# Optimization experiments

Hardware: AMD Instinct MI355X
Metric: run time of the kernel (lower is better)

## Reference

```python
import jax, jax.numpy as jnp
import numpy as np

TASKS = 32768          # init kwarg `tasks`
N_HEADS = TASKS + 1    # tasks + 1 distilled/shared head
IN_DIM, HID, OUT = 3, 100, 5


def setup_inputs() -> dict:
    key = jax.random.key(0)
    kx, k1, kb1, k2, kb2 = jax.random.split(key, 5)
    # per-task stacked parameters (equivalent to ModuleList of Linears)
    x = jax.random.normal(kx, (N_HEADS, IN_DIM), dtype=jnp.float32)
    # init scale ~ PyTorch default: U(-1/sqrt(fan_in), 1/sqrt(fan_in)); gaussian approx fine
    W1 = jax.random.normal(k1, (N_HEADS, HID, IN_DIM), dtype=jnp.float32) * (1.0 / np.sqrt(IN_DIM))
    b1 = jax.random.normal(kb1, (N_HEADS, HID), dtype=jnp.float32) * (1.0 / np.sqrt(IN_DIM))
    W2 = jax.random.normal(k2, (N_HEADS, OUT, HID), dtype=jnp.float32) * (1.0 / np.sqrt(HID))
    b2 = jax.random.normal(kb2, (N_HEADS, OUT), dtype=jnp.float32) * (1.0 / np.sqrt(HID))
    return {"x": x, "W1": W1, "b1": b1, "W2": W2, "b2": b2}


def reference(x, W1, b1, W2, b2):
    # x: (T+1, 3) -- one state vector per task head (matches x.view(tasks+1, -1))
    T1 = W1.shape[0]
    x = x.reshape(T1, -1)                                   # (T+1, 3)
    h = jax.nn.relu(jnp.einsum('thi,ti->th', W1, x) + b1)   # (T+1, 100)
    logits = jnp.einsum('toh,th->to', W2, h) + b2           # (T+1, 5)
    return jax.nn.softmax(logits, axis=-1)                  # (T+1, 5)
```

## Files before the change

### kernel.cpp

```cpp
#include <hip/hip_runtime.h>
#include <math.h>


#define N_HEADS 32769
#define HID     100
#define OUT     5

#define HEADS_PER_BLOCK 4
#define FLOATS_PER_HEAD 400
#define LDS_B1 300

#define GLOBAL_AS __attribute__((address_space(1)))
#define LDS_AS    __attribute__((address_space(3)))

static __device__ __forceinline__ void async_copy16(const void* g, void* l) {
    __builtin_amdgcn_global_load_lds((const GLOBAL_AS void*)g, (LDS_AS void*)l,
                                     16, 0, 0);
}

template <int CTRL, int ROW_MASK>
static __device__ __forceinline__ float dpp_add_step(float acc) {
    union { float f; int i; } in, out;
    in.f = acc;
    out.i = __builtin_amdgcn_update_dpp(0, in.i, CTRL, ROW_MASK, 0xF, false);
    return acc + out.f;
}

static __device__ __forceinline__ float wave_reduce_add(float acc) {
    acc = dpp_add_step<0x111, 0xF>(acc);
    acc = dpp_add_step<0x112, 0xF>(acc);
    acc = dpp_add_step<0x114, 0xF>(acc);
    acc = dpp_add_step<0x118, 0xF>(acc);
    acc = dpp_add_step<0x142, 0xA>(acc);
    acc = dpp_add_step<0x143, 0xC>(acc);
    union { float f; int i; } v, r;
    v.f = acc;
    r.i = __builtin_amdgcn_readlane(v.i, 63);
    return r.f;
}

__global__ __launch_bounds__(256) void distral_kernel(
    const float* __restrict__ x,
    const float* __restrict__ W1,
    const float* __restrict__ b1,
    const float* __restrict__ W2,
    const float* __restrict__ b2,
    float* __restrict__ out)
{
    __shared__ float lds[HEADS_PER_BLOCK * FLOATS_PER_HEAD];

    const int wave = threadIdx.x >> 6;
    const int lane = threadIdx.x & 63;
    const int head = blockIdx.x * HEADS_PER_BLOCK + wave;
    if (head >= N_HEADS) return;

    float* region = lds + wave * FLOATS_PER_HEAD;

    const float* W1h = W1 + (size_t)head * 300;
    const float* b1h = b1 + (size_t)head * 100;
    async_copy16(W1h + 4 * lane,           region);
    if (lane < 11)
        async_copy16(W1h + 256 + 4 * lane, region + 256);
    if (lane < 25)
        async_copy16(b1h + 4 * lane,       region + LDS_B1);

    const float* W2h = W2 + (size_t)head * 500;
    const bool has2 = (lane < HID - 64);

    float w2a[OUT], w2b[OUT] = {0.f, 0.f, 0.f, 0.f, 0.f};
#pragma unroll
    for (int o = 0; o < OUT; ++o)
        w2a[o] = W2h[o * HID + lane];
    if (has2) {
#pragma unroll
        for (int o = 0; o < OUT; ++o)
            w2b[o] = W2h[o * HID + 64 + lane];
    }

    const float x0 = x[head * 3 + 0];
    const float x1 = x[head * 3 + 1];
    const float x2 = x[head * 3 + 2];
    float b2v[OUT];
#pragma unroll
    for (int o = 0; o < OUT; ++o) b2v[o] = b2[head * OUT + o];

    __builtin_amdgcn_s_waitcnt(0x0F70);
    asm volatile("" ::: "memory");

    float h0, h1 = 0.0f;
    {
        const float* r = region + 3 * lane;
        h0 = fmaxf(fmaf(r[0], x0, fmaf(r[1], x1, fmaf(r[2], x2,
                   region[LDS_B1 + lane]))), 0.0f);
    }
    if (has2) {
        const float* r = region + 3 * (lane + 64);
        h1 = fmaxf(fmaf(r[0], x0, fmaf(r[1], x1, fmaf(r[2], x2,
                   region[LDS_B1 + lane + 64]))), 0.0f);
    }

    float logit[OUT];
#pragma unroll
    for (int o = 0; o < OUT; ++o) {
        float p = fmaf(w2b[o], h1, w2a[o] * h0);
        logit[o] = wave_reduce_add(p) + b2v[o];
    }

    float m = -INFINITY;
#pragma unroll
    for (int o = 0; o < OUT; ++o) m = fmaxf(m, logit[o]);
    float e[OUT], s = 0.0f;
#pragma unroll
    for (int o = 0; o < OUT; ++o) { e[o] = __expf(logit[o] - m); s += e[o]; }
    const float inv = 1.0f / s;

    if (lane < OUT) {
        float v = (lane == 0) ? e[0]
                : (lane == 1) ? e[1]
                : (lane == 2) ? e[2]
                : (lane == 3) ? e[3]
                :               e[4];
        out[(size_t)head * OUT + lane] = v * inv;
    }
}

extern "C" void kernel_launch(void* const* d_in, const int* in_sizes, int n_in,
                              void* d_out, int out_size, void* d_ws, size_t ws_size,
                              hipStream_t stream) {
    const float* x  = (const float*)d_in[0];
    const float* W1 = (const float*)d_in[1];
    const float* b1 = (const float*)d_in[2];
    const float* W2 = (const float*)d_in[3];
    const float* b2 = (const float*)d_in[4];
    float* out = (float*)d_out;

    const int blocks = (N_HEADS + HEADS_PER_BLOCK - 1) / HEADS_PER_BLOCK;
    distral_kernel<<<blocks, 256, 0, stream>>>(x, W1, b1, W2, b2, out);
}
```

Baseline: 142.8 us.

## Use persistent waves with register double-buffered prefetch instead of LDS staging

Replaces the one-head-per-wave launch with a fixed grid of 8192 waves that loop over heads, prefetching the next head's weights into registers while the current head is computed. It also drops the LDS async-copy path and loads W1/b1 directly into registers with strided scalar loads. The goal is to hide global memory latency and cut launch and LDS overhead, at the cost of higher register pressure and less coalesced W1 loads (stride-3 per lane).

Result: no change. 145.0 us (+1.5%).

```diff
diff --git a/kernel.cpp b/kernel.cpp
--- a/kernel.cpp
+++ b/kernel.cpp
@@ -5,17 +5,47 @@
 #define N_HEADS 32769
 #define HID     100
 #define OUT     5
+#define NWAVES  8192
 
-#define HEADS_PER_BLOCK 4
-#define FLOATS_PER_HEAD 400
-#define LDS_B1 300
+struct Batch {
+    float w1a0, w1a1, w1a2;
+    float w1b0, w1b1, w1b2;
+    float b1a, b1b;
+    float w2a[OUT], w2b[OUT];
+    float x0, x1, x2;
+    float b2v[OUT];
+};
 
-#define GLOBAL_AS __attribute__((address_space(1)))
-#define LDS_AS    __attribute__((address_space(3)))
+static __device__ __forceinline__ Batch load_batch(
+    const float* __restrict__ x,  const float* __restrict__ W1,
+    const float* __restrict__ b1, const float* __restrict__ W2,
+    const float* __restrict__ b2, int head, int lane)
+{
+    Batch t;
+    const float* W1h = W1 + (size_t)head * 300;
+    const float* b1h = b1 + (size_t)head * 100;
+    const float* W2h = W2 + (size_t)head * 500;
+    const int j2 = (lane + 64 < HID) ? (lane + 64) : (HID - 1);
 
-static __device__ __forceinline__ void async_copy16(const void* g, void* l) {
-    __builtin_amdgcn_global_load_lds((const GLOBAL_AS void*)g, (LDS_AS void*)l,
-                                     16, 0, 0);
+    t.w1a0 = W1h[3 * lane + 0];
+    t.w1a1 = W1h[3 * lane + 1];
+    t.w1a2 = W1h[3 * lane + 2];
+    t.w1b0 = W1h[3 * j2 + 0];
+    t.w1b1 = W1h[3 * j2 + 1];
+    t.w1b2 = W1h[3 * j2 + 2];
+    t.b1a  = b1h[lane];
+    t.b1b  = b1h[j2];
+#pragma unroll
+    for (int o = 0; o < OUT; ++o) {
+        t.w2a[o] = W2h[o * HID + lane];
+        t.w2b[o] = W2h[o * HID + j2];
+    }
+    t.x0 = x[head * 3 + 0];
+    t.x1 = x[head * 3 + 1];
+    t.x2 = x[head * 3 + 2];
+#pragma unroll
+    for (int o = 0; o < OUT; ++o) t.b2v[o] = b2[head * OUT + o];
+    return t;
 }
 
 template <int CTRL, int ROW_MASK>
@@ -39,71 +69,22 @@
     return r.f;
 }
 
-__global__ __launch_bounds__(256) void distral_kernel(
-    const float* __restrict__ x,
-    const float* __restrict__ W1,
-    const float* __restrict__ b1,
-    const float* __restrict__ W2,
-    const float* __restrict__ b2,
-    float* __restrict__ out)
+static __device__ __forceinline__ void process(
+    const Batch& t, int head, int lane, float* __restrict__ out)
 {
-    __shared__ float lds[HEADS_PER_BLOCK * FLOATS_PER_HEAD];
-
-    const int wave = threadIdx.x >> 6;
-    const int lane = threadIdx.x & 63;
-    const int head = blockIdx.x * HEADS_PER_BLOCK + wave;
-    if (head >= N_HEADS) return;
-
-    float* region = lds + wave * FLOATS_PER_HEAD;
-
-    const float* W1h = W1 + (size_t)head * 300;
-    const float* b1h = b1 + (size_t)head * 100;
-    async_copy16(W1h + 4 * lane,           region);
-    if (lane < 11)
-        async_copy16(W1h + 256 + 4 * lane, region + 256);
-    if (lane < 25)
-        async_copy16(b1h + 4 * lane,       region + LDS_B1);
-
-    const float* W2h = W2 + (size_t)head * 500;
     const bool has2 = (lane < HID - 64);
 
-    float w2a[OUT], w2b[OUT] = {0.f, 0.f, 0.f, 0.f, 0.f};
-#pragma unroll
-    for (int o = 0; o < OUT; ++o)
-        w2a[o] = W2h[o * HID + lane];
-    if (has2) {
-#pragma unroll
-        for (int o = 0; o < OUT; ++o)
-            w2b[o] = W2h[o * HID + 64 + lane];
-    }
-
-    const float x0 = x[head * 3 + 0];
-    const float x1 = x[head * 3 + 1];
-    const float x2 = x[head * 3 + 2];
-    float b2v[OUT];
-#pragma unroll
-    for (int o = 0; o < OUT; ++o) b2v[o] = b2[head * OUT + o];
-
-    __builtin_amdgcn_s_waitcnt(0x0F70);
-    asm volatile("" ::: "memory");
-
-    float h0, h1 = 0.0f;
-    {
-        const float* r = region + 3 * lane;
-        h0 = fmaxf(fmaf(r[0], x0, fmaf(r[1], x1, fmaf(r[2], x2,
-                   region[LDS_B1 + lane]))), 0.0f);
-    }
-    if (has2) {
-        const float* r = region + 3 * (lane + 64);
-        h1 = fmaxf(fmaf(r[0], x0, fmaf(r[1], x1, fmaf(r[2], x2,
-                   region[LDS_B1 + lane + 64]))), 0.0f);
-    }
+    float h0 = fmaxf(fmaf(t.w1a0, t.x0, fmaf(t.w1a1, t.x1,
+                     fmaf(t.w1a2, t.x2, t.b1a))), 0.0f);
+    float h1 = fmaxf(fmaf(t.w1b0, t.x0, fmaf(t.w1b1, t.x1,
+                     fmaf(t.w1b2, t.x2, t.b1b))), 0.0f);
+    h1 = has2 ? h1 : 0.0f;
 
     float logit[OUT];
 #pragma unroll
     for (int o = 0; o < OUT; ++o) {
-        float p = fmaf(w2b[o], h1, w2a[o] * h0);
-        logit[o] = wave_reduce_add(p) + b2v[o];
+        float p = fmaf(t.w2b[o], h1, t.w2a[o] * h0);
+        logit[o] = wave_reduce_add(p) + t.b2v[o];
     }
 
     float m = -INFINITY;
@@ -124,6 +105,35 @@
     }
 }
 
+__global__ __launch_bounds__(256) void distral_kernel(
+    const float* __restrict__ x,
+    const float* __restrict__ W1,
+    const float* __restrict__ b1,
+    const float* __restrict__ W2,
+    const float* __restrict__ b2,
+    float* __restrict__ out)
+{
+    const int lane = threadIdx.x & 63;
+    const int w    = (blockIdx.x << 2) | (threadIdx.x >> 6);
+
+    int head  = w;
+    Batch cur = load_batch(x, W1, b1, W2, b2, head, lane);
+
+    for (;;) {
+        const int next  = head + NWAVES;
+        const bool more = (next < N_HEADS);
+        Batch nxt;
+        if (more)
+            nxt = load_batch(x, W1, b1, W2, b2, next, lane);
+
+        process(cur, head, lane, out);
+
+        if (!more) break;
+        cur  = nxt;
+        head = next;
+    }
+}
+
 extern "C" void kernel_launch(void* const* d_in, const int* in_sizes, int n_in,
                               void* d_out, int out_size, void* d_ws, size_t ws_size,
                               hipStream_t stream) {
@@ -134,6 +144,5 @@
     const float* b2 = (const float*)d_in[4];
     float* out = (float*)d_out;
 
-    const int blocks = (N_HEADS + HEADS_PER_BLOCK - 1) / HEADS_PER_BLOCK;
-    distral_kernel<<<blocks, 256, 0, stream>>>(x, W1, b1, W2, b2, out);
+    distral_kernel<<<NWAVES / 4, 256, 0, stream>>>(x, W1, b1, W2, b2, out);
 }
```

## Use persistent waves with double-buffered async LDS staging of all head parameters

Applied to the files above, without the earlier changes.

Replaces the one-head-per-wave launch with a persistent grid of 2816 two-wave blocks. Each wave loops over heads and prefetches the next head's W1, b1, W2, x and b2 into a second LDS buffer while computing the current one. W2, x and b2 now also go through global-to-LDS async copies rather than direct register loads. The aim is to hide memory latency and cut launch and scheduling overhead, at the cost of fewer resident waves, more LDS per wave, and one redundant staging copy on each wave's final iteration.

Result: slower. 146.9 us (+2.9%).

```diff
diff --git a/kernel.cpp b/kernel.cpp
--- a/kernel.cpp
+++ b/kernel.cpp
@@ -6,16 +6,45 @@
 #define HID     100
 #define OUT     5
 
-#define HEADS_PER_BLOCK 4
-#define FLOATS_PER_HEAD 400
-#define LDS_B1 300
+#define WAVES_PER_BLOCK 2
+#define NBLOCKS 2816
+#define NW      (NBLOCKS * WAVES_PER_BLOCK)
+
+#define RSTRIDE 912
+#define OF_B1   300
+#define OF_W2   400
+#define OF_X    900
+#define OF_B2   903
 
 #define GLOBAL_AS __attribute__((address_space(1)))
 #define LDS_AS    __attribute__((address_space(3)))
 
-static __device__ __forceinline__ void async_copy16(const void* g, void* l) {
+static __device__ __forceinline__ void dma16(const void* g, void* l) {
     __builtin_amdgcn_global_load_lds((const GLOBAL_AS void*)g, (LDS_AS void*)l,
                                      16, 0, 0);
+}
+static __device__ __forceinline__ void dma4(const void* g, void* l) {
+    __builtin_amdgcn_global_load_lds((const GLOBAL_AS void*)g, (LDS_AS void*)l,
+                                     4, 0, 0);
+}
+
+static __device__ __forceinline__ void stage_head(
+    int head, int lane, float* region,
+    const float* __restrict__ x,  const float* __restrict__ W1,
+    const float* __restrict__ b1, const float* __restrict__ W2,
+    const float* __restrict__ b2)
+{
+    const float* W1h = W1 + (size_t)head * 300;
+    const float* b1h = b1 + (size_t)head * 100;
+    const float* W2h = W2 + (size_t)head * 500;
+
+    dma16(W1h + 4 * lane,                 region);
+    if (lane < 11) dma16(W1h + 256 + 4 * lane, region + 256);
+    if (lane < 25) dma16(b1h + 4 * lane,  region + OF_B1);
+    dma16(W2h + 4 * lane,                 region + OF_W2);
+    if (lane < 61) dma16(W2h + 256 + 4 * lane, region + OF_W2 + 256);
+    if (lane < 3)  dma4(x + (size_t)head * 3 + lane, region + OF_X);
+    if (lane < 5)  dma4(b2 + (size_t)head * 5 + lane, region + OF_B2);
 }
 
 template <int CTRL, int ROW_MASK>
@@ -25,7 +54,6 @@
     out.i = __builtin_amdgcn_update_dpp(0, in.i, CTRL, ROW_MASK, 0xF, false);
     return acc + out.f;
 }
-
 static __device__ __forceinline__ float wave_reduce_add(float acc) {
     acc = dpp_add_step<0x111, 0xF>(acc);
     acc = dpp_add_step<0x112, 0xF>(acc);
@@ -39,7 +67,7 @@
     return r.f;
 }
 
-__global__ __launch_bounds__(256) void distral_kernel(
+__global__ __launch_bounds__(128) void distral_kernel(
     const float* __restrict__ x,
     const float* __restrict__ W1,
     const float* __restrict__ b1,
@@ -47,80 +75,76 @@
     const float* __restrict__ b2,
     float* __restrict__ out)
 {
-    __shared__ float lds[HEADS_PER_BLOCK * FLOATS_PER_HEAD];
+    __shared__ float lds[WAVES_PER_BLOCK][2][RSTRIDE];
 
-    const int wave = threadIdx.x >> 6;
     const int lane = threadIdx.x & 63;
-    const int head = blockIdx.x * HEADS_PER_BLOCK + wave;
-    if (head >= N_HEADS) return;
+    const int wv   = threadIdx.x >> 6;
+    const int w    = blockIdx.x * WAVES_PER_BLOCK + wv;
 
-    float* region = lds + wave * FLOATS_PER_HEAD;
+    int head = w;
+    stage_head(head, lane, &lds[wv][0][0], x, W1, b1, W2, b2);
 
-    const float* W1h = W1 + (size_t)head * 300;
-    const float* b1h = b1 + (size_t)head * 100;
-    async_copy16(W1h + 4 * lane,           region);
-    if (lane < 11)
-        async_copy16(W1h + 256 + 4 * lane, region + 256);
-    if (lane < 25)
-        async_copy16(b1h + 4 * lane,       region + LDS_B1);
+    int buf = 0;
+    for (;;) {
+        const int  nh   = head + NW;
+        const bool more = (nh < N_HEADS);
+        const int  lh   = more ? nh : w;
+        stage_head(lh, lane, &lds[wv][buf ^ 1][0], x, W1, b1, W2, b2);
 
-    const float* W2h = W2 + (size_t)head * 500;
-    const bool has2 = (lane < HID - 64);
+        asm volatile("" ::: "memory");
+        __builtin_amdgcn_s_waitcnt(0x0F77);
+        asm volatile("" ::: "memory");
 
-    float w2a[OUT], w2b[OUT] = {0.f, 0.f, 0.f, 0.f, 0.f};
+        const float* region = &lds[wv][buf][0];
+
+        const float x0 = region[OF_X + 0];
+        const float x1 = region[OF_X + 1];
+        const float x2 = region[OF_X + 2];
+
+        const bool has2 = (lane < HID - 64);
+        const int  j2   = has2 ? (lane + 64) : (HID - 1);
+
+        float h0, h1;
+        {
+            const float* r = region + 3 * lane;
+            h0 = fmaxf(fmaf(r[0], x0, fmaf(r[1], x1, fmaf(r[2], x2,
+                       region[OF_B1 + lane]))), 0.0f);
+        }
+        {
+            const float* r = region + 3 * j2;
+            h1 = fmaxf(fmaf(r[0], x0, fmaf(r[1], x1, fmaf(r[2], x2,
+                       region[OF_B1 + j2]))), 0.0f);
+            h1 = has2 ? h1 : 0.0f;
+        }
+
+        float logit[OUT];
 #pragma unroll
-    for (int o = 0; o < OUT; ++o)
-        w2a[o] = W2h[o * HID + lane];
-    if (has2) {
+        for (int o = 0; o < OUT; ++o) {
+            float p = fmaf(region[OF_W2 + o * HID + j2], h1,
+                           region[OF_W2 + o * HID + lane] * h0);
+            logit[o] = wave_reduce_add(p) + region[OF_B2 + o];
+        }
+
+        float m = -INFINITY;
 #pragma unroll
-        for (int o = 0; o < OUT; ++o)
-            w2b[o] = W2h[o * HID + 64 + lane];
-    }
+        for (int o = 0; o < OUT; ++o) m = fmaxf(m, logit[o]);
+        float e[OUT], s = 0.0f;
+#pragma unroll
+        for (int o = 0; o < OUT; ++o) { e[o] = __expf(logit[o] - m); s += e[o]; }
+        const float inv = 1.0f / s;
 
-    const float x0 = x[head * 3 + 0];
-    const float x1 = x[head * 3 + 1];
-    const float x2 = x[head * 3 + 2];
-    float b2v[OUT];
-#pragma unroll
-    for (int o = 0; o < OUT; ++o) b2v[o] = b2[head * OUT + o];
+        if (lane < OUT) {
+            float v = (lane == 0) ? e[0]
+                    : (lane == 1) ? e[1]
+                    : (lane == 2) ? e[2]
+                    : (lane == 3) ? e[3]
+                    :               e[4];
+            out[(size_t)head * OUT + lane] = v * inv;
+        }
 
-    __builtin_amdgcn_s_waitcnt(0x0F70);
-    asm volatile("" ::: "memory");
-
-    float h0, h1 = 0.0f;
-    {
-        const float* r = region + 3 * lane;
-        h0 = fmaxf(fmaf(r[0], x0, fmaf(r[1], x1, fmaf(r[2], x2,
-                   region[LDS_B1 + lane]))), 0.0f);
-    }
-    if (has2) {
-        const float* r = region + 3 * (lane + 64);
-        h1 = fmaxf(fmaf(r[0], x0, fmaf(r[1], x1, fmaf(r[2], x2,
-                   region[LDS_B1 + lane + 64]))), 0.0f);
-    }
-
-    float logit[OUT];
-#pragma unroll
-    for (int o = 0; o < OUT; ++o) {
-        float p = fmaf(w2b[o], h1, w2a[o] * h0);
-        logit[o] = wave_reduce_add(p) + b2v[o];
-    }
-
-    float m = -INFINITY;
-#pragma unroll
-    for (int o = 0; o < OUT; ++o) m = fmaxf(m, logit[o]);
-    float e[OUT], s = 0.0f;
-#pragma unroll
-    for (int o = 0; o < OUT; ++o) { e[o] = __expf(logit[o] - m); s += e[o]; }
-    const float inv = 1.0f / s;
-
-    if (lane < OUT) {
-        float v = (lane == 0) ? e[0]
-                : (lane == 1) ? e[1]
-                : (lane == 2) ? e[2]
-                : (lane == 3) ? e[3]
-                :               e[4];
-        out[(size_t)head * OUT + lane] = v * inv;
+        if (!more) break;
+        head = nh;
+        buf ^= 1;
     }
 }
 
@@ -134,6 +158,5 @@
     const float* b2 = (const float*)d_in[4];
     float* out = (float*)d_out;
 
-    const int blocks = (N_HEADS + HEADS_PER_BLOCK - 1) / HEADS_PER_BLOCK;
-    distral_kernel<<<blocks, 256, 0, stream>>>(x, W1, b1, W2, b2, out);
+    distral_kernel<<<NBLOCKS, 128, 0, stream>>>(x, W1, b1, W2, b2, out);
 }
```
